# Kernel tuning notes

Hardware: AMD Instinct MI355X
Metric: run time of the kernel (lower is better)

## Reference

```python
import jax, jax.numpy as jnp
import numpy as np

H = 64
W = 64
DIM = 256          # PatchExpand dim (= out_dim)
EPS = 1e-5         # nn.LayerNorm default eps


def setup_inputs() -> dict:
    key = jax.random.key(0)
    k1, k2 = jax.random.split(key)
    B = 16
    x1 = jax.random.normal(k1, (B, H * W, DIM), dtype=jnp.float32)
    # nn.Linear(dim, 2*dim, bias=False): weight shape [2*dim, dim], y = x @ W.T
    W_expand = jax.random.normal(k2, (2 * DIM, DIM), dtype=jnp.float32) * (1.0 / np.sqrt(DIM))
    ln_gamma = jnp.ones((DIM // 2,), dtype=jnp.float32)
    ln_beta = jnp.zeros((DIM // 2,), dtype=jnp.float32)
    return {"x1": x1, "W_expand": W_expand, "ln_gamma": ln_gamma, "ln_beta": ln_beta}


def _layernorm(x, gamma, beta):
    mu = jnp.mean(x, axis=-1, keepdims=True)
    var = jnp.mean(jnp.square(x - mu), axis=-1, keepdims=True)
    return (x - mu) * jax.lax.rsqrt(var + EPS) * gamma + beta


def reference(x1, W_expand, ln_gamma, ln_beta):
    # MyDecoderLayerDAEFormer.forward with x2=None -> PatchExpand(x1)
    B = x1.shape[0]
    c = DIM // 2
    # Linear expand: [B, H*W, dim] -> [B, H*W, 2*dim]
    x = jnp.einsum('bld,ed->ble', x1, W_expand)
    # b h w (p1 p2 c) -> b (h p1) (w p2) c, p1=p2=2
    x = x.reshape(B, H, W, 2, 2, c)
    x = x.transpose(0, 1, 3, 2, 4, 5).reshape(B, (2 * H) * (2 * W), c)
    return _layernorm(x, ln_gamma, ln_beta)
```

## Files before the change

kernel.cpp:

```cpp
#include <hip/hip_runtime.h>


typedef __attribute__((ext_vector_type(8))) short bf16x8;
typedef __attribute__((ext_vector_type(4))) float f32x4;
typedef __attribute__((ext_vector_type(8))) unsigned short u16x8;

__device__ __forceinline__ unsigned short f2bf(float f) {
    unsigned u = __builtin_bit_cast(unsigned, f);
    u += 0x7fffu + ((u >> 16) & 1u);
    return (unsigned short)(u >> 16);
}

#define GLOAD_LDS16(g, l) __builtin_amdgcn_global_load_lds( \
    (const __attribute__((address_space(1))) unsigned int*)(g), \
    (__attribute__((address_space(3))) unsigned int*)(l), 16, 0, 0)

__global__ void prep_w(const float* __restrict__ Wg, unsigned short* __restrict__ ws) {
    int sg = blockIdx.x * 256 + threadIdx.x;
    int row = sg >> 5;
    int sl  = sg & 31;
    int kc  = sl >> 3;
    int s   = sl & 7;
    const float4* w4 = reinterpret_cast<const float4*>(Wg + (size_t)row * 256 + kc * 64 + s * 8);
    float4 v0 = w4[0], v1 = w4[1];
    u16x8 o = { f2bf(v0.x), f2bf(v0.y), f2bf(v0.z), f2bf(v0.w),
                f2bf(v1.x), f2bf(v1.y), f2bf(v1.z), f2bf(v1.w) };
    char* dst = (char*)ws + kc * 65536 + row * 128 + ((s ^ (row & 7)) << 4);
    *reinterpret_cast<u16x8*>(dst) = o;
}

template <bool WS>
__global__ __launch_bounds__(512, 4)
void fused_expand_ln(const float* __restrict__ x1,
                     const float* __restrict__ Wg,
                     const unsigned short* __restrict__ wbf,
                     const float* __restrict__ gamma,
                     const float* __restrict__ beta,
                     float* __restrict__ out) {
    __shared__ unsigned short Alds[64 * 64];
    __shared__ unsigned short Wlds[512 * 64];

    const int tid  = threadIdx.x;
    const int l0   = blockIdx.x * 64;
    const int wid  = tid >> 6;
    const int lane = tid & 63;
    const int wm   = wid >> 2;
    const int wn   = wid & 3;
    const int g    = lane >> 4;
    const int c    = lane & 15;

    f32x4 acc[2][8];
#pragma unroll
    for (int i = 0; i < 2; ++i)
#pragma unroll
        for (int j = 0; j < 8; ++j) acc[i][j] = (f32x4){0.f, 0.f, 0.f, 0.f};

    for (int kc = 0; kc < 4; ++kc) {
        {
            int row = tid >> 3, s = tid & 7;
            const float4* a4 = reinterpret_cast<const float4*>(
                x1 + (size_t)(l0 + row) * 256 + kc * 64 + s * 8);
            float4 v0 = a4[0], v1 = a4[1];
            u16x8 o = { f2bf(v0.x), f2bf(v0.y), f2bf(v0.z), f2bf(v0.w),
                        f2bf(v1.x), f2bf(v1.y), f2bf(v1.z), f2bf(v1.w) };
            *reinterpret_cast<u16x8*>((char*)Alds + row * 128 + ((s ^ (row & 7)) << 4)) = o;
        }
        if (WS) {
#pragma unroll
            for (int it = 0; it < 8; ++it) {
                const char* gp = (const char*)wbf + kc * 65536 + (tid + it * 512) * 16;
                char* lp = (char*)Wlds + (tid + it * 512) * 16;
                GLOAD_LDS16(gp, lp);
            }
        } else {
#pragma unroll
            for (int j = 0; j < 8; ++j) {
                int fidx = tid + j * 512;
                int row = fidx >> 3, s = fidx & 7;
                const float4* w4 = reinterpret_cast<const float4*>(
                    Wg + (size_t)row * 256 + kc * 64 + s * 8);
                float4 v0 = w4[0], v1 = w4[1];
                u16x8 o = { f2bf(v0.x), f2bf(v0.y), f2bf(v0.z), f2bf(v0.w),
                            f2bf(v1.x), f2bf(v1.y), f2bf(v1.z), f2bf(v1.w) };
                *reinterpret_cast<u16x8*>((char*)Wlds + row * 128 + ((s ^ (row & 7)) << 4)) = o;
            }
        }
        __syncthreads();

#pragma unroll
        for (int ks = 0; ks < 2; ++ks) {
            const int sA = ks * 4 + g;
            bf16x8 a[2];
#pragma unroll
            for (int mi = 0; mi < 2; ++mi) {
                int ra = wm * 32 + mi * 16 + c;
                a[mi] = *reinterpret_cast<const bf16x8*>(
                    (const char*)Alds + ra * 128 + ((sA ^ (ra & 7)) << 4));
            }
#pragma unroll
            for (int ni = 0; ni < 8; ++ni) {
                int rb = wn * 128 + ni * 16 + c;
                bf16x8 b = *reinterpret_cast<const bf16x8*>(
                    (const char*)Wlds + rb * 128 + ((sA ^ (rb & 7)) << 4));
                acc[0][ni] = __builtin_amdgcn_mfma_f32_16x16x32_bf16(a[0], b, acc[0][ni], 0, 0, 0);
                acc[1][ni] = __builtin_amdgcn_mfma_f32_16x16x32_bf16(a[1], b, acc[1][ni], 0, 0, 0);
            }
        }
        __syncthreads();
    }

    const int b  = l0 >> 12;
    const int h  = (l0 & 4095) >> 6;
    const int p1 = wn >> 1, p2 = wn & 1;

    float gam[8], bet[8];
#pragma unroll
    for (int ni = 0; ni < 8; ++ni) {
        gam[ni] = gamma[ni * 16 + c];
        bet[ni] = beta[ni * 16 + c];
    }

    float* outp = out + (size_t)b * (16384 * 128) + (size_t)(2 * h + p1) * (128 * 128);

#pragma unroll
    for (int mi = 0; mi < 2; ++mi) {
#pragma unroll
        for (int r = 0; r < 4; ++r) {
            float s = 0.f, q = 0.f;
#pragma unroll
            for (int ni = 0; ni < 8; ++ni) {
                float v = acc[mi][ni][r];
                s += v; q += v * v;
            }
#pragma unroll
            for (int m = 1; m < 16; m <<= 1) {
                s += __shfl_xor(s, m, 64);
                q += __shfl_xor(q, m, 64);
            }
            const float mean = s * (1.f / 128.f);
            const float var  = q * (1.f / 128.f) - mean * mean;
            const float rstd = rsqrtf(var + 1e-5f);

            const int w = wm * 32 + mi * 16 + g * 4 + r;
            float* orp = outp + (size_t)(2 * w + p2) * 128;
#pragma unroll
            for (int ni = 0; ni < 8; ++ni) {
                float v = (acc[mi][ni][r] - mean) * rstd;
                orp[ni * 16 + c] = v * gam[ni] + bet[ni];
            }
        }
    }
}

extern "C" void kernel_launch(void* const* d_in, const int* in_sizes, int n_in,
                              void* d_out, int out_size, void* d_ws, size_t ws_size,
                              hipStream_t stream) {
    const float* x1  = (const float*)d_in[0];
    const float* Wg  = (const float*)d_in[1];
    const float* gam = (const float*)d_in[2];
    const float* bet = (const float*)d_in[3];
    float* out       = (float*)d_out;

    if (ws_size >= 262144) {
        unsigned short* wbf = (unsigned short*)d_ws;
        hipLaunchKernelGGL(prep_w, dim3(64), dim3(256), 0, stream, Wg, wbf);
        hipLaunchKernelGGL((fused_expand_ln<true>), dim3(1024), dim3(512), 0, stream,
                           x1, Wg, wbf, gam, bet, out);
    } else {
        hipLaunchKernelGGL((fused_expand_ln<false>), dim3(1024), dim3(512), 0, stream,
                           x1, Wg, nullptr, gam, bet, out);
    }
}
```

Baseline: 197.2 us.

## Stream pre-laid-out bf16 weight fragments from global, drop W LDS staging

The weight prep kernel now writes W in MFMA-fragment order, so each lane loads its B operand straight from global/L2 and the 64KB-per-chunk W LDS staging and per-k-chunk barriers are gone. Blocks shrink to 256 threads covering 32 tokens, and the whole 32x256 A tile is converted and staged in LDS once up front. Input loads and output stores use nontemporal hints. In exchange, weights are re-read from L2 by every block and there is no software prefetch of B, so L2 bandwidth and latency may become the limit.

New measurement: 210.7 us. +6.8%, slower.

```diff
diff --git a/kernel.cpp b/kernel.cpp
--- a/kernel.cpp
+++ b/kernel.cpp
@@ -11,43 +11,52 @@
     return (unsigned short)(u >> 16);
 }
 
-#define GLOAD_LDS16(g, l) __builtin_amdgcn_global_load_lds( \
-    (const __attribute__((address_space(1))) unsigned int*)(g), \
-    (__attribute__((address_space(3))) unsigned int*)(l), 16, 0, 0)
-
 __global__ void prep_w(const float* __restrict__ Wg, unsigned short* __restrict__ ws) {
-    int sg = blockIdx.x * 256 + threadIdx.x;
-    int row = sg >> 5;
-    int sl  = sg & 31;
-    int kc  = sl >> 3;
-    int s   = sl & 7;
-    const float4* w4 = reinterpret_cast<const float4*>(Wg + (size_t)row * 256 + kc * 64 + s * 8);
-    float4 v0 = w4[0], v1 = w4[1];
+    int sg  = blockIdx.x * 256 + threadIdx.x;
+    int l   = sg & 63;
+    int fid = sg >> 6;
+    int ks  = fid & 1, ni = (fid >> 1) & 7, wn = (fid >> 4) & 3, kc = fid >> 6;
+    int g = l >> 4, c = l & 15;
+    int row = wn * 128 + ni * 16 + c;
+    int k0  = kc * 64 + ks * 32 + g * 8;
+    const f32x4* w4 = reinterpret_cast<const f32x4*>(Wg + (size_t)row * 256 + k0);
+    f32x4 v0 = w4[0], v1 = w4[1];
     u16x8 o = { f2bf(v0.x), f2bf(v0.y), f2bf(v0.z), f2bf(v0.w),
                 f2bf(v1.x), f2bf(v1.y), f2bf(v1.z), f2bf(v1.w) };
-    char* dst = (char*)ws + kc * 65536 + row * 128 + ((s ^ (row & 7)) << 4);
-    *reinterpret_cast<u16x8*>(dst) = o;
+    *reinterpret_cast<u16x8*>(ws + (size_t)sg * 8) = o;
 }
 
 template <bool WS>
-__global__ __launch_bounds__(512, 4)
+__global__ __launch_bounds__(256, 4)
 void fused_expand_ln(const float* __restrict__ x1,
                      const float* __restrict__ Wg,
                      const unsigned short* __restrict__ wbf,
                      const float* __restrict__ gamma,
                      const float* __restrict__ beta,
                      float* __restrict__ out) {
-    __shared__ unsigned short Alds[64 * 64];
-    __shared__ unsigned short Wlds[512 * 64];
+    __shared__ unsigned short Alds[32 * 256];
 
     const int tid  = threadIdx.x;
-    const int l0   = blockIdx.x * 64;
-    const int wid  = tid >> 6;
+    const int l0   = blockIdx.x * 32;
+    const int wn   = tid >> 6;
     const int lane = tid & 63;
-    const int wm   = wid >> 2;
-    const int wn   = wid & 3;
     const int g    = lane >> 4;
     const int c    = lane & 15;
+
+#pragma unroll
+    for (int j = 0; j < 4; ++j) {
+        int s   = tid + j * 256;
+        int row = s >> 5, sl = s & 31;
+        const f32x4* a4 = reinterpret_cast<const f32x4*>(
+            x1 + (size_t)(l0 + row) * 256 + sl * 8);
+        f32x4 v0 = __builtin_nontemporal_load(a4);
+        f32x4 v1 = __builtin_nontemporal_load(a4 + 1);
+        u16x8 o = { f2bf(v0.x), f2bf(v0.y), f2bf(v0.z), f2bf(v0.w),
+                    f2bf(v1.x), f2bf(v1.y), f2bf(v1.z), f2bf(v1.w) };
+        int sw = (sl & 24) | ((sl & 7) ^ (row & 7));
+        *reinterpret_cast<u16x8*>((char*)Alds + row * 512 + sw * 16) = o;
+    }
+    __syncthreads();
 
     f32x4 acc[2][8];
 #pragma unroll
@@ -55,62 +64,43 @@
 #pragma unroll
         for (int j = 0; j < 8; ++j) acc[i][j] = (f32x4){0.f, 0.f, 0.f, 0.f};
 
+#pragma unroll 1
     for (int kc = 0; kc < 4; ++kc) {
-        {
-            int row = tid >> 3, s = tid & 7;
-            const float4* a4 = reinterpret_cast<const float4*>(
-                x1 + (size_t)(l0 + row) * 256 + kc * 64 + s * 8);
-            float4 v0 = a4[0], v1 = a4[1];
-            u16x8 o = { f2bf(v0.x), f2bf(v0.y), f2bf(v0.z), f2bf(v0.w),
-                        f2bf(v1.x), f2bf(v1.y), f2bf(v1.z), f2bf(v1.w) };
-            *reinterpret_cast<u16x8*>((char*)Alds + row * 128 + ((s ^ (row & 7)) << 4)) = o;
-        }
-        if (WS) {
-#pragma unroll
-            for (int it = 0; it < 8; ++it) {
-                const char* gp = (const char*)wbf + kc * 65536 + (tid + it * 512) * 16;
-                char* lp = (char*)Wlds + (tid + it * 512) * 16;
-                GLOAD_LDS16(gp, lp);
-            }
-        } else {
-#pragma unroll
-            for (int j = 0; j < 8; ++j) {
-                int fidx = tid + j * 512;
-                int row = fidx >> 3, s = fidx & 7;
-                const float4* w4 = reinterpret_cast<const float4*>(
-                    Wg + (size_t)row * 256 + kc * 64 + s * 8);
-                float4 v0 = w4[0], v1 = w4[1];
-                u16x8 o = { f2bf(v0.x), f2bf(v0.y), f2bf(v0.z), f2bf(v0.w),
-                            f2bf(v1.x), f2bf(v1.y), f2bf(v1.z), f2bf(v1.w) };
-                *reinterpret_cast<u16x8*>((char*)Wlds + row * 128 + ((s ^ (row & 7)) << 4)) = o;
-            }
-        }
-        __syncthreads();
-
 #pragma unroll
         for (int ks = 0; ks < 2; ++ks) {
-            const int sA = ks * 4 + g;
+            const int sl3 = ks * 4 + g;
             bf16x8 a[2];
 #pragma unroll
             for (int mi = 0; mi < 2; ++mi) {
-                int ra = wm * 32 + mi * 16 + c;
+                int ra = mi * 16 + c;
                 a[mi] = *reinterpret_cast<const bf16x8*>(
-                    (const char*)Alds + ra * 128 + ((sA ^ (ra & 7)) << 4));
+                    (const char*)Alds + ra * 512 + (kc * 8 | (sl3 ^ (ra & 7))) * 16);
             }
 #pragma unroll
             for (int ni = 0; ni < 8; ++ni) {
-                int rb = wn * 128 + ni * 16 + c;
-                bf16x8 b = *reinterpret_cast<const bf16x8*>(
-                    (const char*)Wlds + rb * 128 + ((sA ^ (rb & 7)) << 4));
+                bf16x8 b;
+                if (WS) {
+                    int fid = ((kc * 4 + wn) * 8 + ni) * 2 + ks;
+                    b = *reinterpret_cast<const bf16x8*>(
+                        wbf + (size_t)fid * 512 + lane * 8);
+                } else {
+                    int rb = wn * 128 + ni * 16 + c;
+                    const f32x4* w4 = reinterpret_cast<const f32x4*>(
+                        Wg + (size_t)rb * 256 + kc * 64 + ks * 32 + g * 8);
+                    f32x4 v0 = w4[0], v1 = w4[1];
+                    u16x8 o = { f2bf(v0.x), f2bf(v0.y), f2bf(v0.z), f2bf(v0.w),
+                                f2bf(v1.x), f2bf(v1.y), f2bf(v1.z), f2bf(v1.w) };
+                    b = __builtin_bit_cast(bf16x8, o);
+                }
                 acc[0][ni] = __builtin_amdgcn_mfma_f32_16x16x32_bf16(a[0], b, acc[0][ni], 0, 0, 0);
                 acc[1][ni] = __builtin_amdgcn_mfma_f32_16x16x32_bf16(a[1], b, acc[1][ni], 0, 0, 0);
             }
         }
-        __syncthreads();
     }
 
     const int b  = l0 >> 12;
-    const int h  = (l0 & 4095) >> 6;
+    const int h  = (l0 >> 6) & 63;
+    const int w0 = l0 & 63;
     const int p1 = wn >> 1, p2 = wn & 1;
 
     float gam[8], bet[8];
@@ -141,12 +131,12 @@
             const float var  = q * (1.f / 128.f) - mean * mean;
             const float rstd = rsqrtf(var + 1e-5f);
 
-            const int w = wm * 32 + mi * 16 + g * 4 + r;
+            const int w = w0 + mi * 16 + g * 4 + r;
             float* orp = outp + (size_t)(2 * w + p2) * 128;
 #pragma unroll
             for (int ni = 0; ni < 8; ++ni) {
                 float v = (acc[mi][ni][r] - mean) * rstd;
-                orp[ni * 16 + c] = v * gam[ni] + bet[ni];
+                __builtin_nontemporal_store(v * gam[ni] + bet[ni], orp + ni * 16 + c);
             }
         }
     }
@@ -164,10 +154,10 @@
     if (ws_size >= 262144) {
         unsigned short* wbf = (unsigned short*)d_ws;
         hipLaunchKernelGGL(prep_w, dim3(64), dim3(256), 0, stream, Wg, wbf);
-        hipLaunchKernelGGL((fused_expand_ln<true>), dim3(1024), dim3(512), 0, stream,
+        hipLaunchKernelGGL((fused_expand_ln<true>), dim3(2048), dim3(256), 0, stream,
                            x1, Wg, wbf, gam, bet, out);
     } else {
-        hipLaunchKernelGGL((fused_expand_ln<false>), dim3(1024), dim3(512), 0, stream,
+        hipLaunchKernelGGL((fused_expand_ln<false>), dim3(2048), dim3(256), 0, stream,
                            x1, Wg, nullptr, gam, bet, out);
     }
 }
```
